# Performance work log

Measured on AMD Instinct MI355X. Metric: run time of the kernel, lower is better.

## Reference

```python
import jax, jax.numpy as jnp
import numpy as np
from jax.ops import segment_sum, segment_max

N_NODES = 50000
N_EDGES = 800000
B = 1024            # number of graphs
NODE_DIM = 21
ESM_DIM = 480
TAB_DIM = 7
H = 128             # hidden_dim
LSTM_H = H // 2     # 64 per direction
NEG_SLOPE = 0.2
BN_EPS = 1e-5


def setup_inputs() -> dict:
    key = jax.random.key(0)
    ks = iter(jax.random.split(key, 48))
    r = lambda shape, s=0.05: (s * jax.random.normal(next(ks), shape)).astype(jnp.float32)
    inp = {
        'x': jax.random.normal(next(ks), (N_NODES, NODE_DIM), dtype=jnp.float32),
        'edge_index': jax.random.randint(next(ks), (2, N_EDGES), 0, N_NODES, dtype=jnp.int64),
        'batch': jnp.sort(jax.random.randint(next(ks), (N_NODES,), 0, B, dtype=jnp.int64)),
        'esm_emb': jax.random.normal(next(ks), (B, ESM_DIM), dtype=jnp.float32),
        'tab_feats': jax.random.normal(next(ks), (B, TAB_DIM), dtype=jnp.float32),
        # GATConv 1 (heads=1)
        'gat1_W': r((H, NODE_DIM)), 'gat1_asrc': r((H,)), 'gat1_adst': r((H,)), 'gat1_b': r((H,)),
        # GATConv 2
        'gat2_W': r((H, H)), 'gat2_asrc': r((H,)), 'gat2_adst': r((H,)), 'gat2_b': r((H,)),
        # Bidirectional LSTM (seq_len=1, so a single cell step per direction)
        'lstm_Wih_f': r((4 * LSTM_H, ESM_DIM)), 'lstm_Whh_f': r((4 * LSTM_H, LSTM_H)),
        'lstm_bih_f': r((4 * LSTM_H,)), 'lstm_bhh_f': r((4 * LSTM_H,)),
        'lstm_Wih_r': r((4 * LSTM_H, ESM_DIM)), 'lstm_Whh_r': r((4 * LSTM_H, LSTM_H)),
        'lstm_bih_r': r((4 * LSTM_H,)), 'lstm_bhh_r': r((4 * LSTM_H,)),
        # tabular net
        'tab_W': r((64, TAB_DIM)), 'tab_b': r((64,)), 'tab_bn_g': jnp.ones((64,), jnp.float32), 'tab_bn_b': jnp.zeros((64,), jnp.float32),
        # fusion head
        'fus1_W': r((256, 320)), 'fus1_b': r((256,)), 'fus_bn_g': jnp.ones((256,), jnp.float32), 'fus_bn_b': jnp.zeros((256,), jnp.float32),
        'fus2_W': r((128, 256)), 'fus2_b': r((128,)),
        'fus3_W': r((1, 128)), 'fus3_b': r((1,)),
    }
    return inp


def _gat(h_in, src, dst, W, a_src, a_dst, bias):
    # PyG GATConv, heads=1, concat=True, self-loops already appended.
    h = h_in @ W.T                                  # [N, H]
    alpha_s = h @ a_src                             # [N]
    alpha_d = h @ a_dst                             # [N]
    e = jax.nn.leaky_relu(alpha_s[src] + alpha_d[dst], NEG_SLOPE)  # [E]
    m = segment_max(e, dst, num_segments=N_NODES)   # stable softmax per target
    ex = jnp.exp(e - m[dst])
    den = segment_sum(ex, dst, num_segments=N_NODES)
    coef = ex / (den[dst] + 1e-16)
    out = segment_sum(coef[:, None] * h[src], dst, num_segments=N_NODES)
    return out + bias


def _bn(x, g, b):
    # BatchNorm1d in training mode: biased batch statistics
    mu = jnp.mean(x, axis=0)
    var = jnp.var(x, axis=0)
    return (x - mu) * jax.lax.rsqrt(var + BN_EPS) * g + b


def _lstm_step(x, Wih, Whh, bih, bhh):
    # single step with zero initial (h, c); Whh term vanishes but kept for fidelity
    g = x @ Wih.T + bih + jnp.zeros((x.shape[0], Whh.shape[1]), x.dtype) @ Whh.T + bhh
    i, f, gg, o = jnp.split(g, 4, axis=1)           # PyTorch gate order i,f,g,o
    c = jax.nn.sigmoid(i) * jnp.tanh(gg)
    return jax.nn.sigmoid(o) * jnp.tanh(c)


def reference(x, edge_index, batch, esm_emb, tab_feats,
              gat1_W, gat1_asrc, gat1_adst, gat1_b,
              gat2_W, gat2_asrc, gat2_adst, gat2_b,
              lstm_Wih_f, lstm_Whh_f, lstm_bih_f, lstm_bhh_f,
              lstm_Wih_r, lstm_Whh_r, lstm_bih_r, lstm_bhh_r,
              tab_W, tab_b, tab_bn_g, tab_bn_b,
              fus1_W, fus1_b, fus_bn_g, fus_bn_b,
              fus2_W, fus2_b, fus3_W, fus3_b):
    sl = jnp.arange(N_NODES, dtype=edge_index.dtype)
    src = jnp.concatenate([edge_index[0], sl])      # add_self_loops=True default
    dst = jnp.concatenate([edge_index[1], sl])

    h1 = jax.nn.relu(_gat(x, src, dst, gat1_W, gat1_asrc, gat1_adst, gat1_b))
    h2 = jax.nn.relu(_gat(h1, src, dst, gat2_W, gat2_asrc, gat2_adst, gat2_b))

    counts = segment_sum(jnp.ones((N_NODES,), h2.dtype), batch, num_segments=B)
    graph_embed = segment_sum(h2, batch, num_segments=B) / jnp.maximum(counts, 1.0)[:, None]

    # bilstm over seq_len=1: output at last (only) step = concat(fwd, bwd)
    h_f = _lstm_step(esm_emb, lstm_Wih_f, lstm_Whh_f, lstm_bih_f, lstm_bhh_f)
    h_r = _lstm_step(esm_emb, lstm_Wih_r, lstm_Whh_r, lstm_bih_r, lstm_bhh_r)
    seq_embed = jnp.concatenate([h_f, h_r], axis=1)  # [B, 128]

    tab_embed = jax.nn.relu(_bn(tab_feats @ tab_W.T + tab_b, tab_bn_g, tab_bn_b))

    z = jnp.concatenate([graph_embed, seq_embed, tab_embed], axis=1)  # [B, 320]
    z = jax.nn.relu(_bn(z @ fus1_W.T + fus1_b, fus_bn_g, fus_bn_b))   # dropout: identity (eval)
    z = jax.nn.relu(z @ fus2_W.T + fus2_b)
    return z @ fus3_W.T + fus3_b                     # [B, 1]
```

## Files before the change

### kernel.cpp

```cpp
#include <hip/hip_runtime.h>
#include <hip/hip_bf16.h>

#define N_NODES 50000
#define N_PAD   50048
#define N_EDGES 800000
#define E_TOT   850000
#define NB      1024
#define ESM_DIM 480
#define HD      128
#define NBUCK   196
#define CAP     5120
#define EPB     3321
#define SC_BLK  256
#define G1_BLK  1563
#define LSTM_BLK 1536
#define BND_BLK 196
#define WC_BLK  16
#define TAB_BLK 4

typedef short short8 __attribute__((ext_vector_type(8)));
typedef unsigned short ushort8 __attribute__((ext_vector_type(8)));
typedef float f32x4 __attribute__((ext_vector_type(4)));

__device__ __forceinline__ float bf2f(unsigned int u) {
    union { unsigned int i; float f; } c; c.i = u << 16; return c.f;
}
__device__ __forceinline__ unsigned short f2bf(float f) {
    union { float f; unsigned int i; } c; c.f = f;
    unsigned int i = c.i;
    return (unsigned short)((i + 0x7FFFu + ((i >> 16) & 1u)) >> 16);
}


__device__ void dev_scatter(const int* __restrict__ ei, int* __restrict__ gcur,
                            int* __restrict__ pairs, int blk) {
    __shared__ int hist[NBUCK];
    int t = threadIdx.x;
    for (int u = t; u < NBUCK; u += 256) hist[u] = 0;
    __syncthreads();
    int e0 = blk * EPB;
    int e1 = (e0 + EPB < E_TOT) ? e0 + EPB : E_TOT;
    for (int e = e0 + t; e < e1; e += 256) {
        int d = (e < N_EDGES) ? ei[N_EDGES + e] : (e - N_EDGES);
        atomicAdd(&hist[d >> 8], 1);
    }
    __syncthreads();
    for (int u = t; u < NBUCK; u += 256) {
        int c = hist[u];
        hist[u] = (c > 0) ? atomicAdd(&gcur[u], c) : 0;
    }
    __syncthreads();
    for (int e = e0 + t; e < e1; e += 256) {
        int s, d;
        if (e < N_EDGES) { s = ei[e]; d = ei[N_EDGES + e]; }
        else             { s = d = e - N_EDGES; }
        int bu = d >> 8;
        int pos = atomicAdd(&hist[bu], 1);
        pairs[bu * CAP + pos] = s | ((d & 255) << 16);
    }
}

__device__ void dev_gat1(const float* __restrict__ X, const float* __restrict__ W,
                         const float* __restrict__ asrc, const float* __restrict__ adst,
                         unsigned short* __restrict__ out,
                         float* __restrict__ alpha_s, float* __restrict__ alpha_d, int blk) {
    __shared__ float Xs[32][23];
    __shared__ float Ws[128][21];
    __shared__ float w_as[21], w_ad[21];
    int t = threadIdx.x;
    int r0 = blk * 32;
    for (int idx = t; idx < 128 * 21; idx += 256) Ws[idx / 21][idx % 21] = W[idx];
    for (int idx = t; idx < 32 * 21; idx += 256) {
        int r = idx / 21, k = idx % 21;
        Xs[r][k] = (r0 + r < N_NODES) ? X[(size_t)(r0 + r) * 21 + k] : 0.f;
    }
    __syncthreads();
    if (t < 21) {
        float sa = 0.f, sd = 0.f;
        for (int f2 = 0; f2 < 128; ++f2) {
            float wv = Ws[f2][t];
            sa += wv * asrc[f2];
            sd += wv * adst[f2];
        }
        w_as[t] = sa; w_ad[t] = sd;
    }
    int f = t & 127, rsub = t >> 7;
    float Wreg[21];
#pragma unroll
    for (int k = 0; k < 21; ++k) Wreg[k] = Ws[f][k];
#pragma unroll 4
    for (int r = rsub; r < 32; r += 2) {
        if (r0 + r >= N_NODES) break;
        float a = 0.f;
#pragma unroll
        for (int k = 0; k < 21; ++k) a += Xs[r][k] * Wreg[k];
        out[(size_t)(r0 + r) * HD + f] = f2bf(a);
    }
    __syncthreads();
    if (t < 32 && r0 + t < N_NODES) {
        float sa = 0.f, sd = 0.f;
#pragma unroll
        for (int k = 0; k < 21; ++k) {
            float xv = Xs[t][k];
            sa += xv * w_as[k];
            sd += xv * w_ad[k];
        }
        alpha_s[r0 + t] = sa;
        alpha_d[r0 + t] = sd;
    }
}

__device__ void dev_gemm_split(const float* __restrict__ X, const float* __restrict__ W1,
                               const float* __restrict__ W2, float* __restrict__ out,
                               int K, int F1, int Ftot, int Kc,
                               int bx, int by, int bz) {
    __shared__ float Xs[16][33];
    __shared__ float Ws[64][33];
    int t = threadIdx.x;
    int r0 = bx * 16;
    int fb = by * 64;
    const float* W = (fb < F1) ? (W1 + (size_t)fb * K) : (W2 + (size_t)(fb - F1) * K);
    int k0 = bz * Kc;
    int f = t & 63, rsub = t >> 6;
    float acc0 = 0.f, acc1 = 0.f, acc2 = 0.f, acc3 = 0.f;
    for (int kc = k0; kc < k0 + Kc; kc += 32) {
        {
            int idx = t * 2, xr = idx >> 5, xk = idx & 31;
            const float2 v = *(const float2*)&X[(size_t)(r0 + xr) * K + kc + xk];
            Xs[xr][xk] = v.x; Xs[xr][xk + 1] = v.y;
        }
        {
            int wf = t >> 2, wk = (t & 3) * 8;
            const float4* p = (const float4*)&W[(size_t)wf * K + kc + wk];
            float4 a = p[0], b = p[1];
            Ws[wf][wk] = a.x; Ws[wf][wk + 1] = a.y; Ws[wf][wk + 2] = a.z; Ws[wf][wk + 3] = a.w;
            Ws[wf][wk + 4] = b.x; Ws[wf][wk + 5] = b.y; Ws[wf][wk + 6] = b.z; Ws[wf][wk + 7] = b.w;
        }
        __syncthreads();
#pragma unroll
        for (int k = 0; k < 32; ++k) {
            float w = Ws[f][k];
            acc0 += Xs[rsub][k] * w;
            acc1 += Xs[rsub + 4][k] * w;
            acc2 += Xs[rsub + 8][k] * w;
            acc3 += Xs[rsub + 12][k] * w;
        }
        __syncthreads();
    }
    atomicAdd(&out[(size_t)(r0 + rsub) * Ftot + fb + f], acc0);
    atomicAdd(&out[(size_t)(r0 + rsub + 4) * Ftot + fb + f], acc1);
    atomicAdd(&out[(size_t)(r0 + rsub + 8) * Ftot + fb + f], acc2);
    atomicAdd(&out[(size_t)(r0 + rsub + 12) * Ftot + fb + f], acc3);
}

__device__ void dev_tab4(const float* __restrict__ tf, const float* __restrict__ W,
                         const float* __restrict__ bias, const float* __restrict__ g,
                         const float* __restrict__ b, float* __restrict__ z, int blk) {
    __shared__ float ssum[16][16];
    __shared__ float ssq[16][16];
    int t = threadIdx.x;
    int rg = t >> 4, jl = t & 15;
    int j = blk * 16 + jl;
    float Wj[7];
#pragma unroll
    for (int k = 0; k < 7; ++k) Wj[k] = W[j * 7 + k];
    float bj = bias[j];
    float s = 0.f, q = 0.f;
    for (int rr = 0; rr < 64; ++rr) {
        int row = rg * 64 + rr;
        const float* xp = &tf[(size_t)row * 7];
        float a = bj;
#pragma unroll
        for (int k = 0; k < 7; ++k) a += xp[k] * Wj[k];
        s += a; q += a * a;
    }
    ssum[rg][jl] = s; ssq[rg][jl] = q;
    __syncthreads();
    for (int off = 8; off; off >>= 1) {
        if (rg < off) { ssum[rg][jl] += ssum[rg + off][jl]; ssq[rg][jl] += ssq[rg + off][jl]; }
        __syncthreads();
    }
    float mu = ssum[0][jl] * (1.f / 1024.f);
    float var = ssq[0][jl] * (1.f / 1024.f) - mu * mu;
    float sc = rsqrtf(var + 1e-5f) * g[j];
    float sh = b[j] - mu * sc;
    for (int rr = 0; rr < 64; ++rr) {
        int row = rg * 64 + rr;
        const float* xp = &tf[(size_t)row * 7];
        float a = bj;
#pragma unroll
        for (int k = 0; k < 7; ++k) a += xp[k] * Wj[k];
        z[(size_t)row * 320 + 256 + j] = fmaxf(a * sc + sh, 0.f);
    }
}

__global__ __launch_bounds__(256) void megaA(
        const int* __restrict__ ei, int* __restrict__ gcur, int* __restrict__ pairs,
        const float* __restrict__ x, const float* __restrict__ gat1_W,
        const float* __restrict__ gat1_as, const float* __restrict__ gat1_ad,
        unsigned short* __restrict__ h0, float* __restrict__ alpha_s, float* __restrict__ alpha_d,
        const float* __restrict__ esm, const float* __restrict__ Wih_f,
        const float* __restrict__ Wih_r, float* __restrict__ g_lstm,
        const int* __restrict__ batch, int* __restrict__ gstart,
        const float* __restrict__ W2, unsigned short* __restrict__ Wb,
        const float* __restrict__ tf, const float* __restrict__ tab_W,
        const float* __restrict__ tab_b, const float* __restrict__ tab_g,
        const float* __restrict__ tab_bb, float* __restrict__ z) {
    int b = blockIdx.x, t = threadIdx.x;
    if (b < SC_BLK) {
        dev_scatter(ei, gcur, pairs, b);
    } else if (b < SC_BLK + G1_BLK) {
        dev_gat1(x, gat1_W, gat1_as, gat1_ad, h0, alpha_s, alpha_d, b - SC_BLK);
    } else if (b < SC_BLK + G1_BLK + LSTM_BLK) {
        int bb = b - (SC_BLK + G1_BLK);
        dev_gemm_split(esm, Wih_f, Wih_r, g_lstm, ESM_DIM, 256, 512, 160,
                       bb & 63, (bb >> 6) & 7, bb >> 9);
    } else if (b < SC_BLK + G1_BLK + LSTM_BLK + BND_BLK) {
        int i = (b - (SC_BLK + G1_BLK + LSTM_BLK)) * 256 + t;
        if (i >= N_NODES) return;
        int bb = batch[i];
        int bp = (i == 0) ? -1 : batch[i - 1];
        for (int g = bp + 1; g <= bb; ++g) gstart[g] = i;
        if (i == N_NODES - 1)
            for (int g = bb + 1; g <= NB; ++g) gstart[g] = N_NODES;
    } else if (b < SC_BLK + G1_BLK + LSTM_BLK + BND_BLK + WC_BLK) {
        int i = (b - (SC_BLK + G1_BLK + LSTM_BLK + BND_BLK)) * 256 + t;
        if (i >= 128 * 32) return;
        float4 v = ((const float4*)W2)[i];
        ((ushort4*)Wb)[i] = make_ushort4(f2bf(v.x), f2bf(v.y), f2bf(v.z), f2bf(v.w));
    } else {
        dev_tab4(tf, tab_W, tab_b, tab_g, tab_bb, z,
                 b - (SC_BLK + G1_BLK + LSTM_BLK + BND_BLK + WC_BLK));
    }
}


__device__ __forceinline__ float sigmoidf_(float x) { return 1.f / (1.f + __expf(-x)); }

__global__ __launch_bounds__(256) void megaB(
        const int* __restrict__ gcur, const int* __restrict__ pairs,
        int* __restrict__ row_beg, int* __restrict__ row_end, int* __restrict__ csr_src,
        const float* __restrict__ g,
        const float* __restrict__ bihf, const float* __restrict__ bhhf,
        const float* __restrict__ bihr, const float* __restrict__ bhhr,
        float* __restrict__ z) {
    int b = blockIdx.x, t = threadIdx.x;
    if (b < NBUCK) {
        __shared__ int dc[256];
        __shared__ int wt[4];
        __shared__ int cur[256];
        int rs = b * CAP;
        int re = rs + gcur[b];
        dc[t] = 0;
        __syncthreads();
        for (int i = rs + t; i < re; i += 256) atomicAdd(&dc[pairs[i] >> 16], 1);
        __syncthreads();
        int v = dc[t];
        int lane = t & 63, wid = t >> 6;
        int sc = v;
#pragma unroll
        for (int off = 1; off < 64; off <<= 1) {
            int n = __shfl_up(sc, off);
            if (lane >= off) sc += n;
        }
        if (lane == 63) wt[wid] = sc;
        __syncthreads();
        int pref = 0;
        for (int ww = 0; ww < wid; ++ww) pref += wt[ww];
        int beg = rs + pref + sc - v;
        int node = b * 256 + t;
        if (node < N_NODES) { row_beg[node] = beg; row_end[node] = beg + v; }
        cur[t] = beg;
        __syncthreads();
        for (int i = rs + t; i < re; i += 256) {
            int pk = pairs[i];
            int pos = atomicAdd(&cur[pk >> 16], 1);
            csr_src[pos] = pk & 0xFFFF;
        }
    } else {
        int idx = (b - NBUCK) * 256 + t;
        if (idx >= NB * 128) return;
        int bb = idx >> 7, jj = idx & 127;
        int dir = jj >> 6, j = jj & 63;
        const float* gb = g + (size_t)bb * 512 + dir * 256;
        const float* bi = dir ? bihr : bihf;
        const float* bh = dir ? bhhr : bhhf;
        float gi = gb[j]       + bi[j]       + bh[j];
        float gg = gb[128 + j] + bi[128 + j] + bh[128 + j];
        float go = gb[192 + j] + bi[192 + j] + bh[192 + j];
        float c = sigmoidf_(gi) * tanhf(gg);
        z[(size_t)bb * 320 + 128 + jj] = sigmoidf_(go) * tanhf(c);
    }
}


__global__ __launch_bounds__(256) void gemm_mfma(const unsigned short* __restrict__ A,
                                                 const unsigned short* __restrict__ Wb,
                                                 const float* __restrict__ asrc,
                                                 const float* __restrict__ adst,
                                                 unsigned short* __restrict__ out,
                                                 float* __restrict__ alpha_s,
                                                 float* __restrict__ alpha_d, int M) {
    __shared__ unsigned short Wlds[128 * 136];
    int t = threadIdx.x;
    for (int u = t; u < 128 * 16; u += 256) {
        int row = u >> 4, seg = u & 15;
        *(ushort8*)&Wlds[row * 136 + seg * 8] = *(const ushort8*)&Wb[row * 128 + seg * 8];
    }
    __syncthreads();
    int wid = t >> 6, L = t & 63;
    int quad = L >> 4, lo = L & 15;
    int m0 = blockIdx.x * 64 + wid * 16;
    short8 afrag[4];
#pragma unroll
    for (int ch = 0; ch < 4; ++ch)
        afrag[ch] = *(const short8*)&A[(size_t)(m0 + lo) * HD + ch * 32 + quad * 8];
    float as_p[4] = {0.f, 0.f, 0.f, 0.f};
    float ad_p[4] = {0.f, 0.f, 0.f, 0.f};
#pragma unroll
    for (int ft = 0; ft < 8; ++ft) {
        f32x4 acc = {0.f, 0.f, 0.f, 0.f};
#pragma unroll
        for (int ch = 0; ch < 4; ++ch) {
            short8 b = *(const short8*)&Wlds[(ft * 16 + lo) * 136 + ch * 32 + quad * 8];
            acc = __builtin_amdgcn_mfma_f32_16x16x32_bf16(afrag[ch], b, acc, 0, 0, 0);
        }
        float asv = asrc[ft * 16 + lo];
        float adv = adst[ft * 16 + lo];
#pragma unroll
        for (int r = 0; r < 4; ++r) {
            int m = m0 + quad * 4 + r;
            if (m < M) out[(size_t)m * HD + ft * 16 + lo] = f2bf(acc[r]);
            as_p[r] += acc[r] * asv;
            ad_p[r] += acc[r] * adv;
        }
    }
#pragma unroll
    for (int off = 1; off < 16; off <<= 1) {
#pragma unroll
        for (int r = 0; r < 4; ++r) {
            as_p[r] += __shfl_xor(as_p[r], off);
            ad_p[r] += __shfl_xor(ad_p[r], off);
        }
    }
    if (lo == 0) {
#pragma unroll
        for (int r = 0; r < 4; ++r) {
            int m = m0 + quad * 4 + r;
            if (m < M) { alpha_s[m] = as_p[r]; alpha_d[m] = ad_p[r]; }
        }
    }
}


__global__ void gat_spmm(const unsigned short* __restrict__ h, const int* __restrict__ row_beg,
                         const int* __restrict__ row_end, const int* __restrict__ csr_src,
                         const float* __restrict__ alpha_s, const float* __restrict__ alpha_d,
                         const float* __restrict__ bias, unsigned short* __restrict__ outp) {
    int w = (int)((blockIdx.x * (size_t)blockDim.x + threadIdx.x) >> 6);
    int lane = threadIdx.x & 63;
    if (w >= N_NODES) return;
    int grp = lane >> 4, l16 = lane & 15;
    int rs = row_beg[w], re = row_end[w];
    int deg = re - rs;
    float ad = alpha_d[w];
    float acc[8] = {0.f, 0.f, 0.f, 0.f, 0.f, 0.f, 0.f, 0.f};
    if (deg <= 64) {
        int s_reg = 0;
        float e = -1e30f;
        if (lane < deg) {
            s_reg = csr_src[rs + lane];
            float t0 = alpha_s[s_reg] + ad;
            e = (t0 > 0.f) ? t0 : 0.2f * t0;
        }
        float m = e;
#pragma unroll
        for (int off = 32; off; off >>= 1) m = fmaxf(m, __shfl_xor(m, off));
        float ex = (lane < deg) ? __expf(e - m) : 0.f;
        float den = ex;
#pragma unroll
        for (int off = 32; off; off >>= 1) den += __shfl_xor(den, off);
        float coef = ex / (den + 1e-16f);
        int i = rs + grp;
        for (; i + 4 < re; i += 8) {
            int idx = i - rs;
            float c0 = __shfl(coef, idx);
            int   s0 = __shfl(s_reg, idx);
            float c1 = __shfl(coef, idx + 4);
            int   s1 = __shfl(s_reg, idx + 4);
            ushort8 h0 = *(const ushort8*)&h[(size_t)s0 * HD + l16 * 8];
            ushort8 h1 = *(const ushort8*)&h[(size_t)s1 * HD + l16 * 8];
#pragma unroll
            for (int j = 0; j < 8; ++j) acc[j] += c0 * bf2f(h0[j]);
#pragma unroll
            for (int j = 0; j < 8; ++j) acc[j] += c1 * bf2f(h1[j]);
        }
        if (i < re) {
            int idx = i - rs;
            float c0 = __shfl(coef, idx);
            int   s0 = __shfl(s_reg, idx);
            ushort8 h0 = *(const ushort8*)&h[(size_t)s0 * HD + l16 * 8];
#pragma unroll
            for (int j = 0; j < 8; ++j) acc[j] += c0 * bf2f(h0[j]);
        }
    } else {
        float m = -1e30f;
        for (int i = rs + lane; i < re; i += 64) {
            int s = csr_src[i];
            float t0 = alpha_s[s] + ad;
            t0 = (t0 > 0.f) ? t0 : 0.2f * t0;
            m = fmaxf(m, t0);
        }
#pragma unroll
        for (int off = 32; off; off >>= 1) m = fmaxf(m, __shfl_xor(m, off));
        float den = 0.f;
        for (int i = rs + lane; i < re; i += 64) {
            int s = csr_src[i];
            float t0 = alpha_s[s] + ad;
            t0 = (t0 > 0.f) ? t0 : 0.2f * t0;
            den += __expf(t0 - m);
        }
#pragma unroll
        for (int off = 32; off; off >>= 1) den += __shfl_xor(den, off);
        float inv = 1.f / (den + 1e-16f);
        for (int i = rs + grp; i < re; i += 4) {
            int s = csr_src[i];
            float t0 = alpha_s[s] + ad;
            t0 = (t0 > 0.f) ? t0 : 0.2f * t0;
            float c = __expf(t0 - m) * inv;
            ushort8 hv = *(const ushort8*)&h[(size_t)s * HD + l16 * 8];
#pragma unroll
            for (int j = 0; j < 8; ++j) acc[j] += c * bf2f(hv[j]);
        }
    }
#pragma unroll
    for (int j = 0; j < 8; ++j) {
        acc[j] += __shfl_xor(acc[j], 16);
        acc[j] += __shfl_xor(acc[j], 32);
    }
    int f0 = l16 * 8 + grp * 2;
    float2 bv = *(const float2*)&bias[f0];
    float vx = fmaxf(acc[grp * 2]     + bv.x, 0.f);
    float vy = fmaxf(acc[grp * 2 + 1] + bv.y, 0.f);
    unsigned int pv = (unsigned int)f2bf(vx) | ((unsigned int)f2bf(vy) << 16);
    *(unsigned int*)&outp[(size_t)w * HD + f0] = pv;
}


__global__ void pool_kernel(const unsigned short* __restrict__ h, const int* __restrict__ start,
                            float* __restrict__ z) {
    int w = (int)((blockIdx.x * (size_t)blockDim.x + threadIdx.x) >> 6);
    int lane = threadIdx.x & 63;
    if (w >= NB) return;
    int grp = lane >> 4, l16 = lane & 15;
    int s0 = start[w], s1 = start[w + 1];
    float acc[8] = {0.f, 0.f, 0.f, 0.f, 0.f, 0.f, 0.f, 0.f};
    int n = s0 + grp;
    for (; n + 4 < s1; n += 8) {
        ushort8 a = *(const ushort8*)&h[(size_t)n * HD + l16 * 8];
        ushort8 b = *(const ushort8*)&h[(size_t)(n + 4) * HD + l16 * 8];
#pragma unroll
        for (int j = 0; j < 8; ++j) acc[j] += bf2f(a[j]);
#pragma unroll
        for (int j = 0; j < 8; ++j) acc[j] += bf2f(b[j]);
    }
    if (n < s1) {
        ushort8 a = *(const ushort8*)&h[(size_t)n * HD + l16 * 8];
#pragma unroll
        for (int j = 0; j < 8; ++j) acc[j] += bf2f(a[j]);
    }
#pragma unroll
    for (int j = 0; j < 8; ++j) {
        acc[j] += __shfl_xor(acc[j], 16);
        acc[j] += __shfl_xor(acc[j], 32);
    }
    float inv = 1.f / fmaxf((float)(s1 - s0), 1.f);
    int f0 = l16 * 8 + grp * 2;
    *(float2*)&z[(size_t)w * 320 + f0] =
        make_float2(acc[grp * 2] * inv, acc[grp * 2 + 1] * inv);
}


__global__ __launch_bounds__(256) void fus1_stats(const float* __restrict__ X,
                                                  const float* __restrict__ W1,
                                                  float* __restrict__ out,
                                                  float* __restrict__ colsum,
                                                  float* __restrict__ colsq) {
    __shared__ float Xs[16][33];
    __shared__ float Ws[64][33];
    __shared__ float cs[4][64];
    __shared__ float cq[4][64];
    int t = threadIdx.x;
    int r0 = blockIdx.x * 16;
    int fb = blockIdx.y * 64;
    const float* W = W1 + (size_t)fb * 320;
    int f = t & 63, rsub = t >> 6;
    float acc0 = 0.f, acc1 = 0.f, acc2 = 0.f, acc3 = 0.f;
    for (int kc = 0; kc < 320; kc += 32) {
        {
            int idx = t * 2, xr = idx >> 5, xk = idx & 31;
            const float2 v = *(const float2*)&X[(size_t)(r0 + xr) * 320 + kc + xk];
            Xs[xr][xk] = v.x; Xs[xr][xk + 1] = v.y;
        }
        {
            int wf = t >> 2, wk = (t & 3) * 8;
            const float4* p = (const float4*)&W[(size_t)wf * 320 + kc + wk];
            float4 a = p[0], b = p[1];
            Ws[wf][wk] = a.x; Ws[wf][wk + 1] = a.y; Ws[wf][wk + 2] = a.z; Ws[wf][wk + 3] = a.w;
            Ws[wf][wk + 4] = b.x; Ws[wf][wk + 5] = b.y; Ws[wf][wk + 6] = b.z; Ws[wf][wk + 7] = b.w;
        }
        __syncthreads();
#pragma unroll
        for (int k = 0; k < 32; ++k) {
            float w = Ws[f][k];
            acc0 += Xs[rsub][k] * w;
            acc1 += Xs[rsub + 4][k] * w;
            acc2 += Xs[rsub + 8][k] * w;
            acc3 += Xs[rsub + 12][k] * w;
        }
        __syncthreads();
    }
    out[(size_t)(r0 + rsub) * 256 + fb + f] = acc0;
    out[(size_t)(r0 + rsub + 4) * 256 + fb + f] = acc1;
    out[(size_t)(r0 + rsub + 8) * 256 + fb + f] = acc2;
    out[(size_t)(r0 + rsub + 12) * 256 + fb + f] = acc3;
    cs[rsub][f] = acc0 + acc1 + acc2 + acc3;
    cq[rsub][f] = acc0 * acc0 + acc1 * acc1 + acc2 * acc2 + acc3 * acc3;
    __syncthreads();
    if (rsub == 0) {
        atomicAdd(&colsum[fb + f], cs[0][f] + cs[1][f] + cs[2][f] + cs[3][f]);
        atomicAdd(&colsq[fb + f],  cq[0][f] + cq[1][f] + cq[2][f] + cq[3][f]);
    }
}


__global__ __launch_bounds__(256) void fus2_final(const float* __restrict__ z1pre,
                                                  const float* __restrict__ colsum,
                                                  const float* __restrict__ colsq,
                                                  const float* __restrict__ fus_g,
                                                  const float* __restrict__ fus_bb,
                                                  const float* __restrict__ W2,
                                                  const float* __restrict__ b2,
                                                  const float* __restrict__ W3,
                                                  const float* __restrict__ b3,
                                                  float* __restrict__ out) {
    __shared__ float Xs[16][33];
    __shared__ float Ws[128][33];
    __shared__ float rowsum[16];
    __shared__ float sc_[256], sh_[256];
    int t = threadIdx.x;
    {
        float mu = colsum[t] * (1.f / 1024.f);
        float var = colsq[t] * (1.f / 1024.f) - mu * mu;
        float s = rsqrtf(var + 1e-5f) * fus_g[t];
        sc_[t] = s;
        sh_[t] = fus_bb[t] - mu * s;
    }
    __syncthreads();
    int r0 = blockIdx.x * 16;
    int f = t & 127, rh = t >> 7;
    float acc[8] = {0.f, 0.f, 0.f, 0.f, 0.f, 0.f, 0.f, 0.f};
    for (int kc = 0; kc < 256; kc += 32) {
        {
            int idx = t * 2, xr = idx >> 5, xk = idx & 31;
            float2 v = *(const float2*)&z1pre[(size_t)(r0 + xr) * 256 + kc + xk];
            Xs[xr][xk]     = fmaxf(v.x * sc_[kc + xk]     + sh_[kc + xk], 0.f);
            Xs[xr][xk + 1] = fmaxf(v.y * sc_[kc + xk + 1] + sh_[kc + xk + 1], 0.f);
        }
#pragma unroll
        for (int i = 0; i < 4; ++i) {
            int id2 = t + 256 * i;
            int wf = id2 >> 3, wk = (id2 & 7) * 4;
            *(float4*)&Ws[wf][wk] = *(const float4*)&W2[(size_t)wf * 256 + kc + wk];
        }
        __syncthreads();
#pragma unroll
        for (int k = 0; k < 32; ++k) {
            float w = Ws[f][k];
#pragma unroll
            for (int r = 0; r < 8; ++r) acc[r] += Xs[rh * 8 + r][k] * w;
        }
        __syncthreads();
    }
    float bv = b2[f], wv = W3[f];
    if (t < 16) rowsum[t] = 0.f;
    __syncthreads();
#pragma unroll
    for (int r = 0; r < 8; ++r) {
        float v = fmaxf(acc[r] + bv, 0.f) * wv;
#pragma unroll
        for (int off = 32; off; off >>= 1) v += __shfl_xor(v, off);
        if ((t & 63) == 0) atomicAdd(&rowsum[rh * 8 + r], v);
    }
    __syncthreads();
    if (t < 16) out[r0 + t] = rowsum[t] + b3[0];
}


extern "C" void kernel_launch(void* const* d_in, const int* in_sizes, int n_in,
                              void* d_out, int out_size, void* d_ws, size_t ws_size,
                              hipStream_t stream) {
    const float* x        = (const float*)d_in[0];
    const int*   ei       = (const int*)d_in[1];
    const int*   batch    = (const int*)d_in[2];
    const float* esm      = (const float*)d_in[3];
    const float* tabf     = (const float*)d_in[4];
    const float* gat1_W   = (const float*)d_in[5];
    const float* gat1_as  = (const float*)d_in[6];
    const float* gat1_ad  = (const float*)d_in[7];
    const float* gat1_b   = (const float*)d_in[8];
    const float* gat2_W   = (const float*)d_in[9];
    const float* gat2_as  = (const float*)d_in[10];
    const float* gat2_ad  = (const float*)d_in[11];
    const float* gat2_b   = (const float*)d_in[12];
    const float* Wih_f    = (const float*)d_in[13];
    const float* bih_f    = (const float*)d_in[15];
    const float* bhh_f    = (const float*)d_in[16];
    const float* Wih_r    = (const float*)d_in[17];
    const float* bih_r    = (const float*)d_in[19];
    const float* bhh_r    = (const float*)d_in[20];
    const float* tab_W    = (const float*)d_in[21];
    const float* tab_b    = (const float*)d_in[22];
    const float* tab_g    = (const float*)d_in[23];
    const float* tab_bb   = (const float*)d_in[24];
    const float* fus1_W   = (const float*)d_in[25];
    const float* fus_g    = (const float*)d_in[27];
    const float* fus_bb   = (const float*)d_in[28];
    const float* fus2_W   = (const float*)d_in[29];
    const float* fus2_b   = (const float*)d_in[30];
    const float* fus3_W   = (const float*)d_in[31];
    const float* fus3_b   = (const float*)d_in[32];
    float* out = (float*)d_out;

    char* ws = (char*)d_ws;
    size_t off = 0;
    auto alloc = [&](size_t bytes) -> char* {
        char* p = ws + off;
        off += (bytes + 255) & ~(size_t)255;
        return p;
    };
    unsigned short* h0_bf = (unsigned short*)alloc((size_t)N_PAD * HD * 2);
    unsigned short* hA_bf = (unsigned short*)alloc((size_t)N_PAD * HD * 2);
    unsigned short* h2_bf = (unsigned short*)alloc((size_t)N_PAD * HD * 2);
    unsigned short* h_act = (unsigned short*)alloc((size_t)N_NODES * HD * 2);
    float* alpha_s = (float*)alloc((size_t)N_NODES * 4);
    float* alpha_d = (float*)alloc((size_t)N_NODES * 4);
    unsigned short* w2bf = (unsigned short*)alloc((size_t)HD * HD * 2);
    int*   row_beg = (int*)alloc((size_t)N_NODES * 4);
    int*   row_end = (int*)alloc((size_t)N_NODES * 4);
    int*   csr_src = (int*)alloc((size_t)NBUCK * CAP * 4);
    int*   pairs   = (int*)alloc((size_t)NBUCK * CAP * 4);
    int*   gstart  = (int*)alloc((size_t)(NB + 1) * 4);
    float* z1pre   = (float*)alloc((size_t)NB * 256 * 4);
    float* z       = (float*)alloc((size_t)NB * 320 * 4);
    float* g_lstm  = (float*)alloc((size_t)NB * 512 * 4);
    int*   gcur    = (int*)alloc((size_t)NBUCK * 4);
    float* colsum  = (float*)alloc((size_t)256 * 4);
    float* colsq   = (float*)alloc((size_t)256 * 4);
    size_t zero_len = (size_t)((char*)colsq + 256 * 4 - (char*)z);
    hipMemsetAsync(z, 0, zero_len, stream);

    megaA<<<SC_BLK + G1_BLK + LSTM_BLK + BND_BLK + WC_BLK + TAB_BLK, 256, 0, stream>>>(
        ei, gcur, pairs, x, gat1_W, gat1_as, gat1_ad, h0_bf, alpha_s, alpha_d,
        esm, Wih_f, Wih_r, g_lstm, batch, gstart, gat2_W, w2bf,
        tabf, tab_W, tab_b, tab_g, tab_bb, z);

    megaB<<<NBUCK + 512, 256, 0, stream>>>(gcur, pairs, row_beg, row_end, csr_src,
                                           g_lstm, bih_f, bhh_f, bih_r, bhh_r, z);

    int aggGrid = (N_NODES + 3) / 4;

    gat_spmm<<<aggGrid, 256, 0, stream>>>(h0_bf, row_beg, row_end, csr_src,
                                          alpha_s, alpha_d, gat1_b, hA_bf);

    gemm_mfma<<<N_PAD / 64, 256, 0, stream>>>(hA_bf, w2bf, gat2_as, gat2_ad,
                                              h2_bf, alpha_s, alpha_d, N_NODES);

    gat_spmm<<<aggGrid, 256, 0, stream>>>(h2_bf, row_beg, row_end, csr_src,
                                          alpha_s, alpha_d, gat2_b, h_act);

    pool_kernel<<<(NB + 3) / 4, 256, 0, stream>>>(h_act, gstart, z);

    fus1_stats<<<dim3(64, 4), 256, 0, stream>>>(z, fus1_W, z1pre, colsum, colsq);

    fus2_final<<<64, 256, 0, stream>>>(z1pre, colsum, colsq, fus_g, fus_bb,
                                       fus2_W, fus2_b, fus3_W, fus3_b, out);

    (void)in_sizes; (void)n_in; (void)out_size; (void)ws_size;
}
```

Measured before the change: 327.3 us.

## Move LSTM input GEMM and GAT1 projection onto split-bf16 MFMA

After: 332.3 us. No clear change (+1.5%).

```diff
diff --git a/kernel.cpp b/kernel.cpp
--- a/kernel.cpp
+++ b/kernel.cpp
@@ -12,11 +12,15 @@
 #define CAP     5120
 #define EPB     3321
 #define SC_BLK  256
-#define G1_BLK  1563
-#define LSTM_BLK 1536
+#define CVT_BLK 256
 #define BND_BLK 196
 #define WC_BLK  16
 #define TAB_BLK 4
+#define G1B     782
+#define LSTM_B  48
+#define LG      384
+#define AGG_GRID 12500
+#define NL_BLK  512
 
 typedef short short8 __attribute__((ext_vector_type(8)));
 typedef unsigned short ushort8 __attribute__((ext_vector_type(8)));
@@ -29,6 +33,10 @@
     union { float f; unsigned int i; } c; c.f = f;
     unsigned int i = c.i;
     return (unsigned short)((i + 0x7FFFu + ((i >> 16) & 1u)) >> 16);
+}
+__device__ __forceinline__ void split2(float v, unsigned short& h, unsigned short& l) {
+    h = f2bf(v);
+    l = f2bf(v - bf2f(h));
 }
 
 
@@ -60,97 +68,40 @@
     }
 }
 
-__device__ void dev_gat1(const float* __restrict__ X, const float* __restrict__ W,
-                         const float* __restrict__ asrc, const float* __restrict__ adst,
-                         unsigned short* __restrict__ out,
-                         float* __restrict__ alpha_s, float* __restrict__ alpha_d, int blk) {
-    __shared__ float Xs[32][23];
-    __shared__ float Ws[128][21];
-    __shared__ float w_as[21], w_ad[21];
-    int t = threadIdx.x;
-    int r0 = blk * 32;
-    for (int idx = t; idx < 128 * 21; idx += 256) Ws[idx / 21][idx % 21] = W[idx];
-    for (int idx = t; idx < 32 * 21; idx += 256) {
-        int r = idx / 21, k = idx % 21;
-        Xs[r][k] = (r0 + r < N_NODES) ? X[(size_t)(r0 + r) * 21 + k] : 0.f;
-    }
-    __syncthreads();
-    if (t < 21) {
-        float sa = 0.f, sd = 0.f;
-        for (int f2 = 0; f2 < 128; ++f2) {
-            float wv = Ws[f2][t];
-            sa += wv * asrc[f2];
-            sd += wv * adst[f2];
-        }
-        w_as[t] = sa; w_ad[t] = sd;
-    }
-    int f = t & 127, rsub = t >> 7;
-    float Wreg[21];
-#pragma unroll
-    for (int k = 0; k < 21; ++k) Wreg[k] = Ws[f][k];
-#pragma unroll 4
-    for (int r = rsub; r < 32; r += 2) {
-        if (r0 + r >= N_NODES) break;
-        float a = 0.f;
-#pragma unroll
-        for (int k = 0; k < 21; ++k) a += Xs[r][k] * Wreg[k];
-        out[(size_t)(r0 + r) * HD + f] = f2bf(a);
-    }
-    __syncthreads();
-    if (t < 32 && r0 + t < N_NODES) {
-        float sa = 0.f, sd = 0.f;
-#pragma unroll
-        for (int k = 0; k < 21; ++k) {
-            float xv = Xs[t][k];
-            sa += xv * w_as[k];
-            sd += xv * w_ad[k];
-        }
-        alpha_s[r0 + t] = sa;
-        alpha_d[r0 + t] = sd;
-    }
-}
-
-__device__ void dev_gemm_split(const float* __restrict__ X, const float* __restrict__ W1,
-                               const float* __restrict__ W2, float* __restrict__ out,
-                               int K, int F1, int Ftot, int Kc,
-                               int bx, int by, int bz) {
-    __shared__ float Xs[16][33];
-    __shared__ float Ws[64][33];
-    int t = threadIdx.x;
-    int r0 = bx * 16;
-    int fb = by * 64;
-    const float* W = (fb < F1) ? (W1 + (size_t)fb * K) : (W2 + (size_t)(fb - F1) * K);
-    int k0 = bz * Kc;
-    int f = t & 63, rsub = t >> 6;
-    float acc0 = 0.f, acc1 = 0.f, acc2 = 0.f, acc3 = 0.f;
-    for (int kc = k0; kc < k0 + Kc; kc += 32) {
-        {
-            int idx = t * 2, xr = idx >> 5, xk = idx & 31;
-            const float2 v = *(const float2*)&X[(size_t)(r0 + xr) * K + kc + xk];
-            Xs[xr][xk] = v.x; Xs[xr][xk + 1] = v.y;
-        }
-        {
-            int wf = t >> 2, wk = (t & 3) * 8;
-            const float4* p = (const float4*)&W[(size_t)wf * K + kc + wk];
-            float4 a = p[0], b = p[1];
-            Ws[wf][wk] = a.x; Ws[wf][wk + 1] = a.y; Ws[wf][wk + 2] = a.z; Ws[wf][wk + 3] = a.w;
-            Ws[wf][wk + 4] = b.x; Ws[wf][wk + 5] = b.y; Ws[wf][wk + 6] = b.z; Ws[wf][wk + 7] = b.w;
-        }
-        __syncthreads();
-#pragma unroll
-        for (int k = 0; k < 32; ++k) {
-            float w = Ws[f][k];
-            acc0 += Xs[rsub][k] * w;
-            acc1 += Xs[rsub + 4][k] * w;
-            acc2 += Xs[rsub + 8][k] * w;
-            acc3 += Xs[rsub + 12][k] * w;
-        }
-        __syncthreads();
-    }
-    atomicAdd(&out[(size_t)(r0 + rsub) * Ftot + fb + f], acc0);
-    atomicAdd(&out[(size_t)(r0 + rsub + 4) * Ftot + fb + f], acc1);
-    atomicAdd(&out[(size_t)(r0 + rsub + 8) * Ftot + fb + f], acc2);
-    atomicAdd(&out[(size_t)(r0 + rsub + 12) * Ftot + fb + f], acc3);
+__device__ void dev_cvt(const float* __restrict__ esm,
+                        const float* __restrict__ Wf,
+                        const float* __restrict__ Wr,
+                        const float* __restrict__ W1,
+                        unsigned short* __restrict__ esm_h, unsigned short* __restrict__ esm_l,
+                        unsigned short* __restrict__ wg_h,  unsigned short* __restrict__ wg_l,
+                        unsigned short* __restrict__ w1h,   unsigned short* __restrict__ w1l,
+                        int blk) {
+    int tid = blk * 256 + threadIdx.x;
+    for (int u = tid; u < NB * 120; u += CVT_BLK * 256) {
+        float4 v = ((const float4*)esm)[u];
+        ushort4 h, l;
+        split2(v.x, h.x, l.x); split2(v.y, h.y, l.y);
+        split2(v.z, h.z, l.z); split2(v.w, h.w, l.w);
+        ((ushort4*)esm_h)[u] = h; ((ushort4*)esm_l)[u] = l;
+    }
+    for (int u = tid; u < LG * 120; u += CVT_BLK * 256) {
+        int n = u / 120, kk = u - n * 120;
+        int rr = (n >= 192) ? n - 192 : n;
+        const float* Ws = (n >= 192) ? Wr : Wf;
+        int srow = (rr < 64) ? rr : rr + 64;
+        float4 v = *(const float4*)&Ws[(size_t)srow * 480 + kk * 4];
+        ushort4 h, l;
+        split2(v.x, h.x, l.x); split2(v.y, h.y, l.y);
+        split2(v.z, h.z, l.z); split2(v.w, h.w, l.w);
+        ((ushort4*)wg_h)[u] = h; ((ushort4*)wg_l)[u] = l;
+    }
+    for (int u = tid; u < 128 * 32; u += CVT_BLK * 256) {
+        int f = u >> 5, k = u & 31;
+        float v = (k < 21) ? W1[f * 21 + k] : 0.f;
+        unsigned short h, l;
+        split2(v, h, l);
+        w1h[u] = h; w1l[u] = l;
+    }
 }
 
 __device__ void dev_tab4(const float* __restrict__ tf, const float* __restrict__ W,
@@ -196,11 +147,11 @@
 
 __global__ __launch_bounds__(256) void megaA(
         const int* __restrict__ ei, int* __restrict__ gcur, int* __restrict__ pairs,
-        const float* __restrict__ x, const float* __restrict__ gat1_W,
-        const float* __restrict__ gat1_as, const float* __restrict__ gat1_ad,
-        unsigned short* __restrict__ h0, float* __restrict__ alpha_s, float* __restrict__ alpha_d,
         const float* __restrict__ esm, const float* __restrict__ Wih_f,
-        const float* __restrict__ Wih_r, float* __restrict__ g_lstm,
+        const float* __restrict__ Wih_r, const float* __restrict__ gat1_W,
+        unsigned short* __restrict__ esm_h, unsigned short* __restrict__ esm_l,
+        unsigned short* __restrict__ wg_h,  unsigned short* __restrict__ wg_l,
+        unsigned short* __restrict__ w1h,   unsigned short* __restrict__ w1l,
         const int* __restrict__ batch, int* __restrict__ gstart,
         const float* __restrict__ W2, unsigned short* __restrict__ Wb,
         const float* __restrict__ tf, const float* __restrict__ tab_W,
@@ -209,41 +160,140 @@
     int b = blockIdx.x, t = threadIdx.x;
     if (b < SC_BLK) {
         dev_scatter(ei, gcur, pairs, b);
-    } else if (b < SC_BLK + G1_BLK) {
-        dev_gat1(x, gat1_W, gat1_as, gat1_ad, h0, alpha_s, alpha_d, b - SC_BLK);
-    } else if (b < SC_BLK + G1_BLK + LSTM_BLK) {
-        int bb = b - (SC_BLK + G1_BLK);
-        dev_gemm_split(esm, Wih_f, Wih_r, g_lstm, ESM_DIM, 256, 512, 160,
-                       bb & 63, (bb >> 6) & 7, bb >> 9);
-    } else if (b < SC_BLK + G1_BLK + LSTM_BLK + BND_BLK) {
-        int i = (b - (SC_BLK + G1_BLK + LSTM_BLK)) * 256 + t;
+    } else if (b < SC_BLK + CVT_BLK) {
+        dev_cvt(esm, Wih_f, Wih_r, gat1_W, esm_h, esm_l, wg_h, wg_l, w1h, w1l, b - SC_BLK);
+    } else if (b < SC_BLK + CVT_BLK + BND_BLK) {
+        int i = (b - (SC_BLK + CVT_BLK)) * 256 + t;
         if (i >= N_NODES) return;
         int bb = batch[i];
         int bp = (i == 0) ? -1 : batch[i - 1];
         for (int g = bp + 1; g <= bb; ++g) gstart[g] = i;
         if (i == N_NODES - 1)
             for (int g = bb + 1; g <= NB; ++g) gstart[g] = N_NODES;
-    } else if (b < SC_BLK + G1_BLK + LSTM_BLK + BND_BLK + WC_BLK) {
-        int i = (b - (SC_BLK + G1_BLK + LSTM_BLK + BND_BLK)) * 256 + t;
+    } else if (b < SC_BLK + CVT_BLK + BND_BLK + WC_BLK) {
+        int i = (b - (SC_BLK + CVT_BLK + BND_BLK)) * 256 + t;
         if (i >= 128 * 32) return;
         float4 v = ((const float4*)W2)[i];
         ((ushort4*)Wb)[i] = make_ushort4(f2bf(v.x), f2bf(v.y), f2bf(v.z), f2bf(v.w));
     } else {
         dev_tab4(tf, tab_W, tab_b, tab_g, tab_bb, z,
-                 b - (SC_BLK + G1_BLK + LSTM_BLK + BND_BLK + WC_BLK));
+                 b - (SC_BLK + CVT_BLK + BND_BLK + WC_BLK));
     }
 }
 
 
 __device__ __forceinline__ float sigmoidf_(float x) { return 1.f / (1.f + __expf(-x)); }
+
+__device__ void dev_gat1_mfma(const float* __restrict__ X,
+                              const unsigned short* __restrict__ w1h,
+                              const unsigned short* __restrict__ w1l,
+                              const float* __restrict__ asrc, const float* __restrict__ adst,
+                              unsigned short* __restrict__ out,
+                              float* __restrict__ alpha_s, float* __restrict__ alpha_d,
+                              int blk) {
+    int t = threadIdx.x;
+    int wid = t >> 6, L = t & 63, quad = L >> 4, lo = L & 15;
+    int m0 = blk * 64 + wid * 16;
+    int row = m0 + lo;
+    const float* xr = X + (size_t)row * 21;
+    int kbase = quad * 8;
+    bool valid = row < N_NODES;
+    float xv[8];
+#pragma unroll
+    for (int j = 0; j < 8; ++j) {
+        int k = kbase + j;
+        xv[j] = (valid && k < 21) ? xr[k] : 0.f;
+    }
+    short8 ah, al;
+#pragma unroll
+    for (int j = 0; j < 8; ++j) {
+        unsigned short h, l;
+        split2(xv[j], h, l);
+        ah[j] = (short)h; al[j] = (short)l;
+    }
+    float as_p[4] = {0.f, 0.f, 0.f, 0.f};
+    float ad_p[4] = {0.f, 0.f, 0.f, 0.f};
+#pragma unroll
+    for (int ft = 0; ft < 8; ++ft) {
+        short8 bh = *(const short8*)&w1h[(ft * 16 + lo) * 32 + kbase];
+        short8 bl = *(const short8*)&w1l[(ft * 16 + lo) * 32 + kbase];
+        f32x4 acc = {0.f, 0.f, 0.f, 0.f};
+        acc = __builtin_amdgcn_mfma_f32_16x16x32_bf16(ah, bh, acc, 0, 0, 0);
+        acc = __builtin_amdgcn_mfma_f32_16x16x32_bf16(al, bh, acc, 0, 0, 0);
+        acc = __builtin_amdgcn_mfma_f32_16x16x32_bf16(ah, bl, acc, 0, 0, 0);
+        float asv = asrc[ft * 16 + lo];
+        float adv = adst[ft * 16 + lo];
+#pragma unroll
+        for (int r = 0; r < 4; ++r) {
+            int m = m0 + quad * 4 + r;
+            out[(size_t)m * HD + ft * 16 + lo] = f2bf(acc[r]);
+            as_p[r] += acc[r] * asv;
+            ad_p[r] += acc[r] * adv;
+        }
+    }
+#pragma unroll
+    for (int off = 1; off < 16; off <<= 1) {
+#pragma unroll
+        for (int r = 0; r < 4; ++r) {
+            as_p[r] += __shfl_xor(as_p[r], off);
+            ad_p[r] += __shfl_xor(ad_p[r], off);
+        }
+    }
+    if (lo == 0) {
+#pragma unroll
+        for (int r = 0; r < 4; ++r) {
+            int m = m0 + quad * 4 + r;
+            if (m < N_NODES) { alpha_s[m] = as_p[r]; alpha_d[m] = ad_p[r]; }
+        }
+    }
+}
+
+__device__ void dev_lstm_mfma(const unsigned short* __restrict__ Ah,
+                              const unsigned short* __restrict__ Al,
+                              const unsigned short* __restrict__ Bh,
+                              const unsigned short* __restrict__ Bl,
+                              float* __restrict__ G, int blk) {
+    int t = threadIdx.x;
+    int wid = t >> 6, L = t & 63, quad = L >> 4, lo = L & 15;
+    int nt = blk % 3, mt = blk / 3;
+    int m0 = mt * 64 + wid * 16;
+    int n0 = nt * 128;
+    f32x4 accs[8];
+#pragma unroll
+    for (int ft = 0; ft < 8; ++ft) accs[ft] = (f32x4){0.f, 0.f, 0.f, 0.f};
+    const unsigned short* arh = Ah + (size_t)(m0 + lo) * ESM_DIM;
+    const unsigned short* arl = Al + (size_t)(m0 + lo) * ESM_DIM;
+    for (int k0 = 0; k0 < ESM_DIM; k0 += 32) {
+        short8 ah = *(const short8*)&arh[k0 + quad * 8];
+        short8 al = *(const short8*)&arl[k0 + quad * 8];
+#pragma unroll
+        for (int ft = 0; ft < 8; ++ft) {
+            size_t boff = (size_t)(n0 + ft * 16 + lo) * ESM_DIM + k0 + quad * 8;
+            short8 bh = *(const short8*)&Bh[boff];
+            short8 bl = *(const short8*)&Bl[boff];
+            accs[ft] = __builtin_amdgcn_mfma_f32_16x16x32_bf16(ah, bh, accs[ft], 0, 0, 0);
+            accs[ft] = __builtin_amdgcn_mfma_f32_16x16x32_bf16(al, bh, accs[ft], 0, 0, 0);
+            accs[ft] = __builtin_amdgcn_mfma_f32_16x16x32_bf16(ah, bl, accs[ft], 0, 0, 0);
+        }
+    }
+#pragma unroll
+    for (int ft = 0; ft < 8; ++ft) {
+#pragma unroll
+        for (int r = 0; r < 4; ++r)
+            G[(size_t)(m0 + quad * 4 + r) * LG + n0 + ft * 16 + lo] = accs[ft][r];
+    }
+}
 
 __global__ __launch_bounds__(256) void megaB(
         const int* __restrict__ gcur, const int* __restrict__ pairs,
         int* __restrict__ row_beg, int* __restrict__ row_end, int* __restrict__ csr_src,
-        const float* __restrict__ g,
-        const float* __restrict__ bihf, const float* __restrict__ bhhf,
-        const float* __restrict__ bihr, const float* __restrict__ bhhr,
-        float* __restrict__ z) {
+        const float* __restrict__ x,
+        const unsigned short* __restrict__ w1h, const unsigned short* __restrict__ w1l,
+        const float* __restrict__ gat1_as, const float* __restrict__ gat1_ad,
+        unsigned short* __restrict__ h0, float* __restrict__ alpha_s, float* __restrict__ alpha_d,
+        const unsigned short* __restrict__ esm_h, const unsigned short* __restrict__ esm_l,
+        const unsigned short* __restrict__ wg_h,  const unsigned short* __restrict__ wg_l,
+        float* __restrict__ g_lstm) {
     int b = blockIdx.x, t = threadIdx.x;
     if (b < NBUCK) {
         __shared__ int dc[256];
@@ -277,19 +327,11 @@
             int pos = atomicAdd(&cur[pk >> 16], 1);
             csr_src[pos] = pk & 0xFFFF;
         }
+    } else if (b < NBUCK + LSTM_B) {
+        dev_lstm_mfma(esm_h, esm_l, wg_h, wg_l, g_lstm, b - NBUCK);
     } else {
-        int idx = (b - NBUCK) * 256 + t;
-        if (idx >= NB * 128) return;
-        int bb = idx >> 7, jj = idx & 127;
-        int dir = jj >> 6, j = jj & 63;
-        const float* gb = g + (size_t)bb * 512 + dir * 256;
-        const float* bi = dir ? bihr : bihf;
-        const float* bh = dir ? bhhr : bhhf;
-        float gi = gb[j]       + bi[j]       + bh[j];
-        float gg = gb[128 + j] + bi[128 + j] + bh[128 + j];
-        float go = gb[192 + j] + bi[192 + j] + bh[192 + j];
-        float c = sigmoidf_(gi) * tanhf(gg);
-        z[(size_t)bb * 320 + 128 + jj] = sigmoidf_(go) * tanhf(c);
+        dev_gat1_mfma(x, w1h, w1l, gat1_as, gat1_ad, h0, alpha_s, alpha_d,
+                      b - (NBUCK + LSTM_B));
     }
 }
 
@@ -356,7 +398,25 @@
 __global__ void gat_spmm(const unsigned short* __restrict__ h, const int* __restrict__ row_beg,
                          const int* __restrict__ row_end, const int* __restrict__ csr_src,
                          const float* __restrict__ alpha_s, const float* __restrict__ alpha_d,
-                         const float* __restrict__ bias, unsigned short* __restrict__ outp) {
+                         const float* __restrict__ bias, unsigned short* __restrict__ outp,
+                         const float* __restrict__ g_lstm,
+                         const float* __restrict__ bihf, const float* __restrict__ bhhf,
+                         const float* __restrict__ bihr, const float* __restrict__ bhhr,
+                         float* __restrict__ z) {
+    if (blockIdx.x >= AGG_GRID) {
+        int idx = (blockIdx.x - AGG_GRID) * 256 + threadIdx.x;
+        int bb = idx >> 7, jj = idx & 127;
+        int dir = jj >> 6, j = jj & 63;
+        const float* gb = g_lstm + (size_t)bb * LG + dir * 192;
+        const float* bi = dir ? bihr : bihf;
+        const float* bh = dir ? bhhr : bhhf;
+        float gi = gb[j]        + bi[j]        + bh[j];
+        float gg = gb[64 + j]   + bi[128 + j]  + bh[128 + j];
+        float go = gb[128 + j]  + bi[192 + j]  + bh[192 + j];
+        float c = sigmoidf_(gi) * tanhf(gg);
+        z[(size_t)bb * 320 + 128 + jj] = sigmoidf_(go) * tanhf(c);
+        return;
+    }
     int w = (int)((blockIdx.x * (size_t)blockDim.x + threadIdx.x) >> 6);
     int lane = threadIdx.x & 63;
     if (w >= N_NODES) return;
@@ -653,31 +713,40 @@
     int*   gstart  = (int*)alloc((size_t)(NB + 1) * 4);
     float* z1pre   = (float*)alloc((size_t)NB * 256 * 4);
     float* z       = (float*)alloc((size_t)NB * 320 * 4);
-    float* g_lstm  = (float*)alloc((size_t)NB * 512 * 4);
+    float* g_lstm  = (float*)alloc((size_t)NB * LG * 4);
+    unsigned short* esm_h = (unsigned short*)alloc((size_t)NB * ESM_DIM * 2);
+    unsigned short* esm_l = (unsigned short*)alloc((size_t)NB * ESM_DIM * 2);
+    unsigned short* wg_h  = (unsigned short*)alloc((size_t)LG * ESM_DIM * 2);
+    unsigned short* wg_l  = (unsigned short*)alloc((size_t)LG * ESM_DIM * 2);
+    unsigned short* w1h   = (unsigned short*)alloc((size_t)128 * 32 * 2);
+    unsigned short* w1l   = (unsigned short*)alloc((size_t)128 * 32 * 2);
     int*   gcur    = (int*)alloc((size_t)NBUCK * 4);
     float* colsum  = (float*)alloc((size_t)256 * 4);
     float* colsq   = (float*)alloc((size_t)256 * 4);
-    size_t zero_len = (size_t)((char*)colsq + 256 * 4 - (char*)z);
-    hipMemsetAsync(z, 0, zero_len, stream);
-
-    megaA<<<SC_BLK + G1_BLK + LSTM_BLK + BND_BLK + WC_BLK + TAB_BLK, 256, 0, stream>>>(
-        ei, gcur, pairs, x, gat1_W, gat1_as, gat1_ad, h0_bf, alpha_s, alpha_d,
-        esm, Wih_f, Wih_r, g_lstm, batch, gstart, gat2_W, w2bf,
+    size_t zero_len = (size_t)((char*)colsq + 256 * 4 - (char*)gcur);
+    hipMemsetAsync(gcur, 0, zero_len, stream);
+
+    megaA<<<SC_BLK + CVT_BLK + BND_BLK + WC_BLK + TAB_BLK, 256, 0, stream>>>(
+        ei, gcur, pairs, esm, Wih_f, Wih_r, gat1_W,
+        esm_h, esm_l, wg_h, wg_l, w1h, w1l,
+        batch, gstart, gat2_W, w2bf,
         tabf, tab_W, tab_b, tab_g, tab_bb, z);
 
-    megaB<<<NBUCK + 512, 256, 0, stream>>>(gcur, pairs, row_beg, row_end, csr_src,
-                                           g_lstm, bih_f, bhh_f, bih_r, bhh_r, z);
-
-    int aggGrid = (N_NODES + 3) / 4;
-
-    gat_spmm<<<aggGrid, 256, 0, stream>>>(h0_bf, row_beg, row_end, csr_src,
-                                          alpha_s, alpha_d, gat1_b, hA_bf);
+    megaB<<<NBUCK + LSTM_B + G1B, 256, 0, stream>>>(
+        gcur, pairs, row_beg, row_end, csr_src,
+        x, w1h, w1l, gat1_as, gat1_ad, h0_bf, alpha_s, alpha_d,
+        esm_h, esm_l, wg_h, wg_l, g_lstm);
+
+    gat_spmm<<<AGG_GRID + NL_BLK, 256, 0, stream>>>(h0_bf, row_beg, row_end, csr_src,
+                                                    alpha_s, alpha_d, gat1_b, hA_bf,
+                                                    g_lstm, bih_f, bhh_f, bih_r, bhh_r, z);
 
     gemm_mfma<<<N_PAD / 64, 256, 0, stream>>>(hA_bf, w2bf, gat2_as, gat2_ad,
                                               h2_bf, alpha_s, alpha_d, N_NODES);
 
-    gat_spmm<<<aggGrid, 256, 0, stream>>>(h2_bf, row_beg, row_end, csr_src,
-                                          alpha_s, alpha_d, gat2_b, h_act);
+    gat_spmm<<<AGG_GRID, 256, 0, stream>>>(h2_bf, row_beg, row_end, csr_src,
+                                           alpha_s, alpha_d, gat2_b, h_act,
+                                           g_lstm, bih_f, bhh_f, bih_r, bhh_r, z);
 
     pool_kernel<<<(NB + 3) / 4, 256, 0, stream>>>(h_act, gstart, z);
 
```
